# Performance work log

Hardware: AMD Instinct MI355X
Metric: run time of the kernel (lower is better)

Reference implementation:

```python
import jax, jax.numpy as jnp
import numpy as np

N_HEAD = 32
N_KV = 8
HEAD_DIM = 64  # n_embd // n_head = 2048 // 32
EPS = 1e-6


def bit_linear(x, w):
    """BitNet b1.58 BitLinear (no bias): int8 absmax activation quant (per-token),
    ternary mean-absmax weight quant, straight-through estimator."""
    s = 127.0 / jnp.clip(jnp.max(jnp.abs(x), axis=-1, keepdims=True), 1e-5)
    xq = jnp.clip(jnp.round(x * s), -128.0, 127.0) / s
    xq = x + jax.lax.stop_gradient(xq - x)
    ws = 1.0 / jnp.clip(jnp.mean(jnp.abs(w)), 1e-5)
    wq = jnp.clip(jnp.round(w * ws), -1.0, 1.0) / ws
    wq = w + jax.lax.stop_gradient(wq - w)
    return xq @ wq.T


def sub_ln(x, gamma, beta):
    mean = jnp.mean(x, axis=-1, keepdims=True)
    var = jnp.mean((x - mean) ** 2, axis=-1, keepdims=True)
    return (x - mean) / jnp.sqrt(var + EPS) * gamma + beta


def setup_inputs() -> dict:
    key = jax.random.key(0)
    ks = jax.random.split(key, 8)
    D, KV, F = 2048, 512, 8192
    B, T = 1, 2048
    w_scale = 0.02
    return {
        "x": jax.random.normal(ks[0], (B, T, D), jnp.float32),
        "g1": jnp.ones((D,), jnp.float32),
        "b1": jnp.zeros((D,), jnp.float32),
        "g2": jnp.ones((D,), jnp.float32),
        "b2": jnp.zeros((D,), jnp.float32),
        "wq": jax.random.normal(ks[1], (D, D), jnp.float32) * w_scale,
        "wk": jax.random.normal(ks[2], (KV, D), jnp.float32) * w_scale,
        "wv": jax.random.normal(ks[3], (KV, D), jnp.float32) * w_scale,
        "wo": jax.random.normal(ks[4], (D, D), jnp.float32) * w_scale,
        "w1": jax.random.normal(ks[5], (F, D), jnp.float32) * w_scale,
        "w2": jax.random.normal(ks[6], (D, F), jnp.float32) * w_scale,
    }


def reference(x, g1, b1, g2, b2, wq, wk, wv, wo, w1, w2):
    B, T, D = x.shape
    # --- attention sublayer (pre-norm, residual) ---
    h = sub_ln(x, g1, b1)
    q = bit_linear(h, wq).reshape(B, T, N_HEAD, HEAD_DIM)
    k = bit_linear(h, wk).reshape(B, T, N_KV, HEAD_DIM)
    v = bit_linear(h, wv).reshape(B, T, N_KV, HEAD_DIM)
    rep = N_HEAD // N_KV
    k = jnp.repeat(k, rep, axis=2)  # GQA repeat_interleave
    v = jnp.repeat(v, rep, axis=2)
    attn = jnp.einsum('bqhd,bkhd->bhqk', q, k) * (HEAD_DIM ** -0.5)
    causal = jnp.tril(jnp.ones((T, T), bool))
    attn = jnp.where(causal, attn, -jnp.inf)
    attn = jax.nn.softmax(attn, axis=-1)
    o = jnp.einsum('bhqk,bkhd->bqhd', attn, v).reshape(B, T, D)
    x = x + bit_linear(o, wo)
    # --- FFN sublayer (pre-norm, residual, ReLU^2) ---
    h2 = sub_ln(x, g2, b2)
    f = bit_linear(h2, w1)
    f = jnp.maximum(f, 0.0) ** 2
    return x + bit_linear(f, w2)
```

## Files before the change

kernel.cpp:

```cpp
#include <hip/hip_runtime.h>
#include <hip/hip_bf16.h>
#include <stdint.h>

typedef __bf16 bf16;
typedef signed char i8;
typedef __bf16 v8bf __attribute__((ext_vector_type(8)));
typedef __bf16 v4bf __attribute__((ext_vector_type(4)));
typedef signed char v8i8 __attribute__((ext_vector_type(8)));
typedef int    v4i  __attribute__((ext_vector_type(4)));
typedef float  f32x16 __attribute__((ext_vector_type(16)));

#define MFMA32(a,b,c)   __builtin_amdgcn_mfma_f32_32x32x16_bf16((a),(b),(c),0,0,0)
#define MFMA_I8(a,b,c)  __builtin_amdgcn_mfma_i32_16x16x64_i8((a),(b),(c),0,0,0)

__device__ __forceinline__ void glds16(const void* g, void* l) {
  __builtin_amdgcn_global_load_lds(
      (const __attribute__((address_space(1))) void*)g,
      (__attribute__((address_space(3))) void*)l, 16, 0, 0);
}

__device__ __forceinline__ float wred_sum(float v) {
#pragma unroll
  for (int o = 32; o; o >>= 1) v += __shfl_xor(v, o);
  return v;
}
__device__ __forceinline__ float wred_max(float v) {
#pragma unroll
  for (int o = 32; o; o >>= 1) v = fmaxf(v, __shfl_xor(v, o));
  return v;
}

__device__ __forceinline__ unsigned int packbf(float a, float b) {
  union { bf16 h[2]; unsigned int u; } x;
  x.h[0] = (bf16)a; x.h[1] = (bf16)b;
  return x.u;
}

__global__ void k_sniff(const unsigned short* __restrict__ x, int* __restrict__ flag) {
  int cnt = 0;
  for (int i = threadIdx.x; i < 2048; i += 64) {
    const unsigned short u = x[i];
    const int e = (u >> 7) & 0xFF;
    if (u == 0 || (e >= 100 && e <= 140)) cnt++;
  }
#pragma unroll
  for (int o = 32; o; o >>= 1) cnt += __shfl_xor(cnt, o);
  if (threadIdx.x == 0) flag[0] = (cnt >= 1844) ? 0 : 1;
}


__global__ void k_zero(float* p, int n) {
  int i = threadIdx.x;
  if (i < n) p[i] = 0.0f;
}

__global__ __launch_bounds__(256) void k_zerof(float4* __restrict__ p) {
  p[(size_t)blockIdx.x * 256 + threadIdx.x] = make_float4(0.f, 0.f, 0.f, 0.f);
}

__global__ __launch_bounds__(256) void k_abssum(const void* __restrict__ w, int n,
                                                const int* __restrict__ flag,
                                                float* __restrict__ out) {
  const int tid = threadIdx.x;
  const int f32 = flag[0];
  __shared__ float sred[4];
  float s = 0.0f;
  if (f32) {
    const float4* p = (const float4*)w;
    for (int i = (blockIdx.x * 256 + tid) * 2; i * 4 < n; i += gridDim.x * 512) {
      float4 a = p[i], b = p[i + 1];
      s += fabsf(a.x) + fabsf(a.y) + fabsf(a.z) + fabsf(a.w) +
           fabsf(b.x) + fabsf(b.y) + fabsf(b.z) + fabsf(b.w);
    }
  } else {
    const bf16* p = (const bf16*)w;
    for (int i = (blockIdx.x * 256 + tid) * 8; i < n; i += gridDim.x * 2048) {
      v8bf v = *(const v8bf*)(p + i);
#pragma unroll
      for (int j = 0; j < 8; j++) s += fabsf((float)v[j]);
    }
  }
  s = wred_sum(s);
  if ((tid & 63) == 0) sred[tid >> 6] = s;
  __syncthreads();
  if (tid == 0) atomicAdd(out, sred[0] + sred[1] + sred[2] + sred[3]);
}

__global__ __launch_bounds__(256) void k_wquant(const void* __restrict__ w, i8* __restrict__ o,
                                                const float* __restrict__ sum, float invn,
                                                const int* __restrict__ flag) {
  const int gid = blockIdx.x * 256 + threadIdx.x;
  const int i = gid * 8;
  const float ws = 1.0f / fmaxf(sum[0] * invn, 1e-5f);
  const int f32 = flag[0];
  float v[8];
  if (f32) {
    float4 a = ((const float4*)w)[gid * 2];
    float4 b = ((const float4*)w)[gid * 2 + 1];
    v[0] = a.x; v[1] = a.y; v[2] = a.z; v[3] = a.w;
    v[4] = b.x; v[5] = b.y; v[6] = b.z; v[7] = b.w;
  } else {
    v8bf t = *(const v8bf*)((const bf16*)w + i);
#pragma unroll
    for (int j = 0; j < 8; j++) v[j] = (float)t[j];
  }
  v8i8 r;
#pragma unroll
  for (int j = 0; j < 8; j++) {
    float t = rintf(v[j] * ws);
    r[j] = (i8)fminf(fmaxf(t, -1.0f), 1.0f);
  }
  *(v8i8*)(o + i) = r;
}

template <bool XINT>
__global__ __launch_bounds__(256) void k_lnq(const void* __restrict__ x, const void* __restrict__ g,
                                             const void* __restrict__ b, i8* __restrict__ q,
                                             float* __restrict__ sc, const int* __restrict__ flag) {
  const int row = blockIdx.x, tid = threadIdx.x;
  const int f32 = flag[0];
  __shared__ float sred[4];
  float v[8];
#pragma unroll
  for (int i = 0; i < 8; i++) {
    const size_t idx = (size_t)row * 2048 + tid + 256 * i;
    if (XINT)      v[i] = ((const float*)x)[idx];
    else if (f32)  v[i] = ((const float*)x)[idx];
    else           v[i] = (float)((const bf16*)x)[idx];
  }
  float s = 0.0f;
#pragma unroll
  for (int i = 0; i < 8; i++) s += v[i];
  s = wred_sum(s);
  if ((tid & 63) == 0) sred[tid >> 6] = s;
  __syncthreads();
  const float mean = (sred[0] + sred[1] + sred[2] + sred[3]) * (1.0f / 2048.0f);
  __syncthreads();
  float vs = 0.0f;
#pragma unroll
  for (int i = 0; i < 8; i++) { float d = v[i] - mean; vs += d * d; }
  vs = wred_sum(vs);
  if ((tid & 63) == 0) sred[tid >> 6] = vs;
  __syncthreads();
  const float rstd = rsqrtf((sred[0] + sred[1] + sred[2] + sred[3]) * (1.0f / 2048.0f) + 1e-6f);
  __syncthreads();
  float hq[8];
  float am = 0.0f;
#pragma unroll
  for (int i = 0; i < 8; i++) {
    const int c = tid + 256 * i;
    const float gv = f32 ? ((const float*)g)[c] : (float)((const bf16*)g)[c];
    const float bv = f32 ? ((const float*)b)[c] : (float)((const bf16*)b)[c];
    hq[i] = (v[i] - mean) * rstd * gv + bv;
    am = fmaxf(am, fabsf(hq[i]));
  }
  am = wred_max(am);
  if ((tid & 63) == 0) sred[tid >> 6] = am;
  __syncthreads();
  am = fmaxf(fmaxf(sred[0], sred[1]), fmaxf(sred[2], sred[3]));
  const float cl = fmaxf(am, 1e-5f);
  const float s127 = 127.0f / cl;
#pragma unroll
  for (int i = 0; i < 8; i++) {
    float r = rintf(hq[i] * s127);
    r = fminf(fmaxf(r, -128.0f), 127.0f);
    q[(size_t)row * 2048 + tid + 256 * i] = (i8)r;
  }
  if (tid == 0) sc[row] = cl * (1.0f / 127.0f);
}

template <int IT>
__global__ __launch_bounds__(256) void k_rowq(const bf16* __restrict__ in, i8* __restrict__ q,
                                              float* __restrict__ sc) {
  const int row = blockIdx.x, tid = threadIdx.x;
  const int C = IT * 256;
  __shared__ float sred[4];
  const bf16* xr = in + (size_t)row * C;
  float v[IT];
  float am = 0.0f;
#pragma unroll
  for (int i = 0; i < IT; i++) {
    v[i] = (float)xr[tid + 256 * i];
    am = fmaxf(am, fabsf(v[i]));
  }
  am = wred_max(am);
  if ((tid & 63) == 0) sred[tid >> 6] = am;
  __syncthreads();
  am = fmaxf(fmaxf(sred[0], sred[1]), fmaxf(sred[2], sred[3]));
  const float cl = fmaxf(am, 1e-5f);
  const float s127 = 127.0f / cl;
#pragma unroll
  for (int i = 0; i < IT; i++) {
    float r = rintf(v[i] * s127);
    r = fminf(fmaxf(r, -128.0f), 127.0f);
    q[(size_t)row * C + tid + 256 * i] = (i8)r;
  }
  if (tid == 0) sc[row] = cl * (1.0f / 127.0f);
}

template <int EPI>
__global__ __launch_bounds__(256) void k_gemm(const i8* __restrict__ A, const i8* __restrict__ B,
                                              const float* __restrict__ sA,
                                              const float* __restrict__ wsum, float winv,
                                              void* __restrict__ out,
                                              int M, int N, int K, int Kc,
                                              const int* __restrict__ flag) {
  __shared__ __align__(16) i8 As[128 * 64];
  __shared__ __align__(16) i8 Bs[128 * 64];
  const int tid = threadIdx.x;
  const int lane = tid & 63;
  const int ml = lane & 15;
  const int q4 = lane >> 4;
  const int wid = tid >> 6;
  const int wM = wid >> 1;
  const int wN = wid & 1;
  const int m0 = blockIdx.y * 128;
  const int n0 = blockIdx.x * 128;

  const int r0 = tid >> 2;
  const int c0 = (tid & 3) * 16;
  const i8* Ag0 = A + (size_t)(m0 + r0) * K + c0;
  const i8* Ag1 = Ag0 + (size_t)64 * K;
  const i8* Bg0 = B + (size_t)(n0 + r0) * K + c0;
  const i8* Bg1 = Bg0 + (size_t)64 * K;
  i8* as0 = &As[wid * 1024];
  i8* as1 = &As[4096 + wid * 1024];
  i8* bs0 = &Bs[wid * 1024];
  i8* bs1 = &Bs[4096 + wid * 1024];

  v4i acc[4][4] = {};

  const int kbeg = blockIdx.z * Kc;
  const int kfin = kbeg + Kc;
  for (int k0 = kbeg; k0 < kfin; k0 += 64) {
    __syncthreads();
    glds16(Ag0 + k0, as0);
    glds16(Ag1 + k0, as1);
    glds16(Bg0 + k0, bs0);
    glds16(Bg1 + k0, bs1);
    __syncthreads();
    v4i af[4], bfr[4];
#pragma unroll
    for (int i = 0; i < 4; i++) af[i] = *(const v4i*)&As[(wM * 64 + i * 16 + ml) * 64 + q4 * 16];
#pragma unroll
    for (int j = 0; j < 4; j++) bfr[j] = *(const v4i*)&Bs[(wN * 64 + j * 16 + ml) * 64 + q4 * 16];
#pragma unroll
    for (int i = 0; i < 4; i++)
#pragma unroll
      for (int j = 0; j < 4; j++) acc[i][j] = MFMA_I8(af[i], bfr[j], acc[i][j]);
  }

  if (EPI == 4) {
    int* ob = (int*)out;
#pragma unroll
    for (int i = 0; i < 4; i++)
#pragma unroll
      for (int r = 0; r < 4; r++) {
        const int row = m0 + wM * 64 + i * 16 + q4 * 4 + r;
#pragma unroll
        for (int j = 0; j < 4; j++) {
          const int col = n0 + wN * 64 + j * 16 + ml;
          atomicAdd(ob + (size_t)row * N + col, acc[i][j][r]);
        }
      }
    return;
  }

  const float cw = fmaxf(wsum[0] * winv, 1e-5f);
#pragma unroll
  for (int i = 0; i < 4; i++) {
#pragma unroll
    for (int r = 0; r < 4; r++) {
      const int row = m0 + wM * 64 + i * 16 + q4 * 4 + r;
      const float sa = sA[row] * cw;
#pragma unroll
      for (int j = 0; j < 4; j++) {
        const int col = n0 + wN * 64 + j * 16 + ml;
        const float val = (float)acc[i][j][r] * sa;
        float u = fmaxf(val, 0.0f);
        ((bf16*)out)[(size_t)row * N + col] = (bf16)(u * u);
      }
    }
  }
}

template <int MODE>
__global__ __launch_bounds__(256) void k_epi(const int* __restrict__ acc, int lda, int cofs,
                                             int ncols,
                                             const float* __restrict__ sA,
                                             const float* __restrict__ wsum, float winv,
                                             const void* __restrict__ resid,
                                             void* __restrict__ out,
                                             const int* __restrict__ flag) {
  const int row = blockIdx.x, tid = threadIdx.x;
  const float cw = fmaxf(wsum[0] * winv, 1e-5f);
  const float srow = (MODE == 3) ? cw : sA[row] * cw;
  const int f32 = flag[0];
  for (int c = tid * 4; c < ncols; c += 1024) {
    const v4i a = *(const v4i*)(acc + (size_t)row * lda + cofs + c);
    float s0 = srow, s1 = srow, s2 = srow, s3 = srow;
    if (MODE == 3) {
      float4 sc = *(const float4*)(sA + c);
      s0 *= sc.x; s1 *= sc.y; s2 *= sc.z; s3 *= sc.w;
    }
    const float v0 = (float)a[0] * s0, v1 = (float)a[1] * s1;
    const float v2 = (float)a[2] * s2, v3 = (float)a[3] * s3;
    const size_t o = (size_t)row * ncols + c;
    if (MODE == 0 || MODE == 3) {
      v4bf r;
      r[0] = (bf16)v0; r[1] = (bf16)v1; r[2] = (bf16)v2; r[3] = (bf16)v3;
      *(v4bf*)((bf16*)out + o) = r;
    } else if (MODE == 1) {
      float4 rv;
      if (f32) {
        rv = *(const float4*)((const float*)resid + o);
      } else {
        const v4bf rb = *(const v4bf*)((const bf16*)resid + o);
        rv = make_float4((float)rb[0], (float)rb[1], (float)rb[2], (float)rb[3]);
      }
      *(float4*)((float*)out + o) = make_float4(rv.x + v0, rv.y + v1, rv.z + v2, rv.w + v3);
    } else {
      const float4 rv = *(const float4*)((const float*)resid + o);
      const float o0 = rv.x + v0, o1 = rv.y + v1, o2 = rv.z + v2, o3 = rv.w + v3;
      if (f32) {
        *(float4*)((float*)out + o) = make_float4(o0, o1, o2, o3);
      } else {
        v4bf r;
        r[0] = (bf16)o0; r[1] = (bf16)o1; r[2] = (bf16)o2; r[3] = (bf16)o3;
        *(v4bf*)((bf16*)out + o) = r;
      }
    }
  }
}

__global__ __launch_bounds__(64) void k_attn(const bf16* __restrict__ Q, const bf16* __restrict__ Kb,
                                             const bf16* __restrict__ Vt, bf16* __restrict__ O) {
  const int h = blockIdx.y;
  const int kvh = h >> 2;
  const int t = (blockIdx.x + ((h >> 2) << 3)) & 63;
  const int qw0 = t * 32;
  const int lane = threadIdx.x;
  const int ql = lane & 31;
  const int hi = lane >> 5;

  v8bf qf[4];
  {
    const bf16* qp = Q + (size_t)(qw0 + ql) * 2048 + h * 64 + hi * 8;
#pragma unroll
    for (int c = 0; c < 4; c++) qf[c] = *(const v8bf*)(qp + c * 16);
  }

  float m = -1e30f, l = 0.0f;
  f32x16 acc0 = {}, acc1 = {};

  const bf16* kbase = Kb + kvh * 64 + hi * 8;
  const bf16* vbase = Vt + (size_t)(kvh * 64 + ql) * 2048 + hi * 8;

  for (int kb = 0; kb <= qw0; kb += 32) {
    f32x16 s = {};
    {
      const bf16* kp = kbase + (size_t)(kb + ql) * 512;
#pragma unroll
      for (int c = 0; c < 4; c++) {
        const v8bf kf = *(const v8bf*)(kp + c * 16);
        s = MFMA32(kf, qf[c], s);
      }
    }
    const bool diag = (kb == qw0);
    float p[16];
    float rm = -1e30f;
#pragma unroll
    for (int r = 0; r < 16; r++) {
      float v = s[r] * 0.125f;
      const int koff = (r & 3) + ((r >> 2) << 3) + (hi << 2);
      if (diag && koff > ql) v = -1e30f;
      p[r] = v;
      rm = fmaxf(rm, v);
    }
    rm = fmaxf(rm, __shfl_xor(rm, 32));
    const float mn = fmaxf(m, rm);
    const float alpha = __expf(m - mn);
    m = mn;
    float rs = 0.0f;
#pragma unroll
    for (int r = 0; r < 16; r++) {
      p[r] = __expf(p[r] - mn);
      rs += p[r];
    }
    rs += __shfl_xor(rs, 32);
    l = l * alpha + rs;
#pragma unroll
    for (int r = 0; r < 16; r++) { acc0[r] *= alpha; acc1[r] *= alpha; }

    unsigned int w0 = packbf(p[0], p[1]),   w2 = packbf(p[4], p[5]);
    unsigned int w1 = packbf(p[2], p[3]),   w3 = packbf(p[6], p[7]);
    unsigned int x0 = packbf(p[8], p[9]),   x2 = packbf(p[12], p[13]);
    unsigned int x1 = packbf(p[10], p[11]), x3 = packbf(p[14], p[15]);
    asm("v_permlane32_swap_b32 %0, %1" : "+v"(w0), "+v"(w2));
    asm("v_permlane32_swap_b32 %0, %1" : "+v"(w1), "+v"(w3));
    asm("v_permlane32_swap_b32 %0, %1" : "+v"(x0), "+v"(x2));
    asm("v_permlane32_swap_b32 %0, %1" : "+v"(x1), "+v"(x3));
    union BU { unsigned int u[4]; v8bf v; } B0, B1;
    B0.u[0] = w0; B0.u[1] = w1; B0.u[2] = w2; B0.u[3] = w3;
    B1.u[0] = x0; B1.u[1] = x1; B1.u[2] = x2; B1.u[3] = x3;

    const bf16* vp = vbase + kb;
    const v8bf v00 = *(const v8bf*)(vp);
    const v8bf v01 = *(const v8bf*)(vp + 16);
    const v8bf v10 = *(const v8bf*)(vp + (size_t)32 * 2048);
    const v8bf v11 = *(const v8bf*)(vp + (size_t)32 * 2048 + 16);
    acc0 = MFMA32(v00, B0.v, acc0);
    acc0 = MFMA32(v01, B1.v, acc0);
    acc1 = MFMA32(v10, B0.v, acc1);
    acc1 = MFMA32(v11, B1.v, acc1);
  }

  const float inv = 1.0f / l;
  unsigned int* op = (unsigned int*)(O + (size_t)(qw0 + ql) * 2048 + h * 64);
#pragma unroll
  for (int r = 0; r < 16; r += 2) {
    const int d = (r & 3) + ((r >> 2) << 3) + (hi << 2);
    op[d >> 1] = packbf(acc0[r] * inv, acc0[r + 1] * inv);
    op[(d >> 1) + 16] = packbf(acc1[r] * inv, acc1[r + 1] * inv);
  }
}

extern "C" void kernel_launch(void* const* d_in, const int* in_sizes, int n_in, void* d_out,
                              int out_size, void* d_ws, size_t ws_size, hipStream_t stream) {
  const void* x = d_in[0];
  const void* g1 = d_in[1];
  const void* b1 = d_in[2];
  const void* g2 = d_in[3];
  const void* b2 = d_in[4];
  const void* wq = d_in[5];
  const void* wk = d_in[6];
  const void* wv = d_in[7];
  const void* wo = d_in[8];
  const void* w1 = d_in[9];
  const void* w2 = d_in[10];

  char* ws = (char*)d_ws;
  const size_t MB = 1ull << 20;
  float* wsum = (float*)ws;
  float* s1 = (float*)(ws + 8192);
  float* so = (float*)(ws + 16384);
  float* s2 = (float*)(ws + 24576);
  float* sf = (float*)(ws + 32768);
  int* flag = (int*)(ws + 40960);
  char* big = ws + 65536;

  i8* w1z = (i8*)(big);
  i8* fq  = (i8*)(big);
  i8* w2z = (i8*)(big + 16 * MB);
  i8* wqz = (i8*)(big + 32 * MB);
  i8* wkz = (i8*)(big + 36 * MB);
  i8* wvz = (i8*)(big + 37 * MB);
  i8* woz = (i8*)(big + 38 * MB);
  i8* xq1 = (i8*)(big + 42 * MB);
  i8* oq  = xq1;
  i8* xq2 = xq1;
  int* accQK = (int*)(big + 46 * MB);
  int* accO  = (int*)(big + 46 * MB);
  bf16* Fb   = (bf16*)(big + 46 * MB);
  int* accF  = (int*)(big + 46 * MB);
  int* accVt = (int*)(big + 66 * MB);
  bf16* Qb   = (bf16*)(big + 70 * MB);
  bf16* Kbuf = (bf16*)(big + 78 * MB);
  bf16* Vt   = (bf16*)(big + 80 * MB);
  bf16* Ob   = (bf16*)(big + 82 * MB);
  float* x1  = (float*)(big + 78 * MB);

  const float invD2 = 1.0f / 4194304.0f;
  const float invKV = 1.0f / 1048576.0f;
  const float invF = 1.0f / 16777216.0f;

  k_sniff<<<1, 64, 0, stream>>>((const unsigned short*)x, flag);
  k_zero<<<1, 64, 0, stream>>>(wsum, 8);
  k_zerof<<<6144, 256, 0, stream>>>((float4*)accQK);

  k_abssum<<<512, 256, 0, stream>>>(wq, 2048 * 2048, flag, wsum + 0);
  k_abssum<<<512, 256, 0, stream>>>(wk, 512 * 2048, flag, wsum + 1);
  k_abssum<<<512, 256, 0, stream>>>(wv, 512 * 2048, flag, wsum + 2);
  k_abssum<<<512, 256, 0, stream>>>(wo, 2048 * 2048, flag, wsum + 3);
  k_abssum<<<512, 256, 0, stream>>>(w1, 8192 * 2048, flag, wsum + 4);
  k_abssum<<<512, 256, 0, stream>>>(w2, 2048 * 8192, flag, wsum + 5);
  k_wquant<<<2048, 256, 0, stream>>>(wq, wqz, wsum + 0, invD2, flag);
  k_wquant<<<512, 256, 0, stream>>>(wk, wkz, wsum + 1, invKV, flag);
  k_wquant<<<512, 256, 0, stream>>>(wv, wvz, wsum + 2, invKV, flag);
  k_wquant<<<2048, 256, 0, stream>>>(wo, woz, wsum + 3, invD2, flag);
  k_wquant<<<8192, 256, 0, stream>>>(w1, w1z, wsum + 4, invF, flag);
  k_wquant<<<8192, 256, 0, stream>>>(w2, w2z, wsum + 5, invF, flag);

  k_lnq<false><<<2048, 256, 0, stream>>>(x, g1, b1, xq1, s1, flag);
  k_gemm<4><<<dim3(20, 16, 4), 256, 0, stream>>>(xq1, wqz, s1, wsum + 0, invD2, accQK,
                                                 2048, 2560, 2048, 512, flag);
  k_gemm<4><<<dim3(16, 4, 4), 256, 0, stream>>>(wvz, xq1, s1, wsum + 2, invKV, accVt,
                                                512, 2048, 2048, 512, flag);
  k_epi<0><<<2048, 256, 0, stream>>>(accQK, 2560, 0, 2048, s1, wsum + 0, invD2, nullptr, Qb, flag);
  k_epi<0><<<2048, 256, 0, stream>>>(accQK, 2560, 2048, 512, s1, wsum + 1, invKV, nullptr, Kbuf, flag);
  k_epi<3><<<512, 256, 0, stream>>>(accVt, 2048, 0, 2048, s1, wsum + 2, invKV, nullptr, Vt, flag);
  k_attn<<<dim3(64, 32), 64, 0, stream>>>(Qb, Kbuf, Vt, Ob);
  k_rowq<8><<<2048, 256, 0, stream>>>(Ob, oq, so);
  k_zerof<<<4096, 256, 0, stream>>>((float4*)accO);
  k_gemm<4><<<dim3(16, 16, 4), 256, 0, stream>>>(oq, woz, so, wsum + 3, invD2, accO,
                                                 2048, 2048, 2048, 512, flag);
  k_epi<1><<<2048, 256, 0, stream>>>(accO, 2048, 0, 2048, so, wsum + 3, invD2, x, x1, flag);

  k_lnq<true><<<2048, 256, 0, stream>>>(x1, g2, b2, xq2, s2, flag);
  k_gemm<2><<<dim3(64, 16, 1), 256, 0, stream>>>(xq2, w1z, s2, wsum + 4, invF, Fb,
                                                 2048, 8192, 2048, 2048, flag);
  k_rowq<32><<<2048, 256, 0, stream>>>(Fb, fq, sf);
  k_zerof<<<4096, 256, 0, stream>>>((float4*)accF);
  k_gemm<4><<<dim3(16, 16, 4), 256, 0, stream>>>(fq, w2z, sf, wsum + 5, invF, accF,
                                                 2048, 2048, 8192, 2048, flag);
  k_epi<2><<<2048, 256, 0, stream>>>(accF, 2048, 0, 2048, sf, wsum + 5, invF, x1, d_out, flag);
}
```

Baseline: 715.8 us.

## Batch weight abs-sum and quant launches, double-buffer int8 GEMM LDS tiles

The six per-weight abs-sum launches become one kernel, and the six ternary-quant launches become another. Each kernel picks its weight segment from the block index, which removes launch overhead and small-grid tails. The int8 MFMA GEMM now uses two LDS buffers, so the next K tile's global-to-LDS load is issued before computing on the current tile, dropping one barrier per iteration. Workspace offsets are rearranged so the FFN buffers reuse dead regions. The cost is doubled LDS use per block, which may reduce occupancy.

```diff
diff --git a/kernel.cpp b/kernel.cpp
--- a/kernel.cpp
+++ b/kernel.cpp
@@ -13,6 +13,10 @@
 #define MFMA32(a,b,c)   __builtin_amdgcn_mfma_f32_32x32x16_bf16((a),(b),(c),0,0,0)
 #define MFMA_I8(a,b,c)  __builtin_amdgcn_mfma_i32_16x16x64_i8((a),(b),(c),0,0,0)
 
+#define INV_D2 (1.0f / 4194304.0f)
+#define INV_KV (1.0f / 1048576.0f)
+#define INV_F  (1.0f / 16777216.0f)
+
 __device__ __forceinline__ void glds16(const void* g, void* l) {
   __builtin_amdgcn_global_load_lds(
       (const __attribute__((address_space(1))) void*)g,
@@ -58,24 +62,33 @@
   p[(size_t)blockIdx.x * 256 + threadIdx.x] = make_float4(0.f, 0.f, 0.f, 0.f);
 }
 
-__global__ __launch_bounds__(256) void k_abssum(const void* __restrict__ w, int n,
-                                                const int* __restrict__ flag,
-                                                float* __restrict__ out) {
-  const int tid = threadIdx.x;
+__global__ __launch_bounds__(256) void k_abssum6(const void* __restrict__ p0, const void* __restrict__ p1,
+                                                 const void* __restrict__ p2, const void* __restrict__ p3,
+                                                 const void* __restrict__ p4, const void* __restrict__ p5,
+                                                 const int* __restrict__ flag, float* __restrict__ out) {
+  const int b = blockIdx.x, tid = threadIdx.x;
+  const void* w; int seg, base;
+  if (b < 64)       { w = p0; seg = 0; base = b; }
+  else if (b < 80)  { w = p1; seg = 1; base = b - 64; }
+  else if (b < 96)  { w = p2; seg = 2; base = b - 80; }
+  else if (b < 160) { w = p3; seg = 3; base = b - 96; }
+  else if (b < 416) { w = p4; seg = 4; base = b - 160; }
+  else              { w = p5; seg = 5; base = b - 416; }
   const int f32 = flag[0];
   __shared__ float sred[4];
   float s = 0.0f;
   if (f32) {
-    const float4* p = (const float4*)w;
-    for (int i = (blockIdx.x * 256 + tid) * 2; i * 4 < n; i += gridDim.x * 512) {
-      float4 a = p[i], b = p[i + 1];
-      s += fabsf(a.x) + fabsf(a.y) + fabsf(a.z) + fabsf(a.w) +
-           fabsf(b.x) + fabsf(b.y) + fabsf(b.z) + fabsf(b.w);
+    const float4* p = (const float4*)w + (size_t)base * 16384;
+#pragma unroll 4
+    for (int i = 0; i < 64; i++) {
+      float4 a = p[i * 256 + tid];
+      s += fabsf(a.x) + fabsf(a.y) + fabsf(a.z) + fabsf(a.w);
     }
   } else {
-    const bf16* p = (const bf16*)w;
-    for (int i = (blockIdx.x * 256 + tid) * 8; i < n; i += gridDim.x * 2048) {
-      v8bf v = *(const v8bf*)(p + i);
+    const v8bf* p = (const v8bf*)w + (size_t)base * 8192;
+#pragma unroll 4
+    for (int i = 0; i < 32; i++) {
+      v8bf v = p[i * 256 + tid];
 #pragma unroll
       for (int j = 0; j < 8; j++) s += fabsf((float)v[j]);
     }
@@ -83,22 +96,35 @@
   s = wred_sum(s);
   if ((tid & 63) == 0) sred[tid >> 6] = s;
   __syncthreads();
-  if (tid == 0) atomicAdd(out, sred[0] + sred[1] + sred[2] + sred[3]);
-}
-
-__global__ __launch_bounds__(256) void k_wquant(const void* __restrict__ w, i8* __restrict__ o,
-                                                const float* __restrict__ sum, float invn,
-                                                const int* __restrict__ flag) {
-  const int gid = blockIdx.x * 256 + threadIdx.x;
+  if (tid == 0) atomicAdd(out + seg, sred[0] + sred[1] + sred[2] + sred[3]);
+}
+
+__global__ __launch_bounds__(256) void k_wquant6(const void* __restrict__ p0, const void* __restrict__ p1,
+                                                 const void* __restrict__ p2, const void* __restrict__ p3,
+                                                 const void* __restrict__ p4, const void* __restrict__ p5,
+                                                 i8* __restrict__ d0, i8* __restrict__ d1,
+                                                 i8* __restrict__ d2, i8* __restrict__ d3,
+                                                 i8* __restrict__ d4, i8* __restrict__ d5,
+                                                 const float* __restrict__ wsum,
+                                                 const int* __restrict__ flag) {
+  const int b = blockIdx.x;
+  const void* w; i8* o; int seg, base; float invn;
+  if (b < 2048)       { w = p0; o = d0; seg = 0; base = b;         invn = INV_D2; }
+  else if (b < 2560)  { w = p1; o = d1; seg = 1; base = b - 2048;  invn = INV_KV; }
+  else if (b < 3072)  { w = p2; o = d2; seg = 2; base = b - 2560;  invn = INV_KV; }
+  else if (b < 5120)  { w = p3; o = d3; seg = 3; base = b - 3072;  invn = INV_D2; }
+  else if (b < 13312) { w = p4; o = d4; seg = 4; base = b - 5120;  invn = INV_F; }
+  else                { w = p5; o = d5; seg = 5; base = b - 13312; invn = INV_F; }
+  const int gid = base * 256 + threadIdx.x;
   const int i = gid * 8;
-  const float ws = 1.0f / fmaxf(sum[0] * invn, 1e-5f);
+  const float ws = 1.0f / fmaxf(wsum[seg] * invn, 1e-5f);
   const int f32 = flag[0];
   float v[8];
   if (f32) {
     float4 a = ((const float4*)w)[gid * 2];
-    float4 b = ((const float4*)w)[gid * 2 + 1];
+    float4 b4 = ((const float4*)w)[gid * 2 + 1];
     v[0] = a.x; v[1] = a.y; v[2] = a.z; v[3] = a.w;
-    v[4] = b.x; v[5] = b.y; v[6] = b.z; v[7] = b.w;
+    v[4] = b4.x; v[5] = b4.y; v[6] = b4.z; v[7] = b4.w;
   } else {
     v8bf t = *(const v8bf*)((const bf16*)w + i);
 #pragma unroll
@@ -205,8 +231,8 @@
                                               void* __restrict__ out,
                                               int M, int N, int K, int Kc,
                                               const int* __restrict__ flag) {
-  __shared__ __align__(16) i8 As[128 * 64];
-  __shared__ __align__(16) i8 Bs[128 * 64];
+  __shared__ __align__(16) i8 As[2][128 * 64];
+  __shared__ __align__(16) i8 Bs[2][128 * 64];
   const int tid = threadIdx.x;
   const int lane = tid & 63;
   const int ml = lane & 15;
@@ -223,31 +249,38 @@
   const i8* Ag1 = Ag0 + (size_t)64 * K;
   const i8* Bg0 = B + (size_t)(n0 + r0) * K + c0;
   const i8* Bg1 = Bg0 + (size_t)64 * K;
-  i8* as0 = &As[wid * 1024];
-  i8* as1 = &As[4096 + wid * 1024];
-  i8* bs0 = &Bs[wid * 1024];
-  i8* bs1 = &Bs[4096 + wid * 1024];
+  const int l0 = wid * 1024;
+  const int l1 = 4096 + wid * 1024;
 
   v4i acc[4][4] = {};
 
   const int kbeg = blockIdx.z * Kc;
   const int kfin = kbeg + Kc;
+  glds16(Ag0 + kbeg, &As[0][l0]);
+  glds16(Ag1 + kbeg, &As[0][l1]);
+  glds16(Bg0 + kbeg, &Bs[0][l0]);
+  glds16(Bg1 + kbeg, &Bs[0][l1]);
+  __syncthreads();
+  int cb = 0;
   for (int k0 = kbeg; k0 < kfin; k0 += 64) {
+    const int kn = k0 + 64;
+    if (kn < kfin) {
+      glds16(Ag0 + kn, &As[cb ^ 1][l0]);
+      glds16(Ag1 + kn, &As[cb ^ 1][l1]);
+      glds16(Bg0 + kn, &Bs[cb ^ 1][l0]);
+      glds16(Bg1 + kn, &Bs[cb ^ 1][l1]);
+    }
+    v4i af[4], bfr[4];
+#pragma unroll
+    for (int i = 0; i < 4; i++) af[i] = *(const v4i*)&As[cb][(wM * 64 + i * 16 + ml) * 64 + q4 * 16];
+#pragma unroll
+    for (int j = 0; j < 4; j++) bfr[j] = *(const v4i*)&Bs[cb][(wN * 64 + j * 16 + ml) * 64 + q4 * 16];
+#pragma unroll
+    for (int i = 0; i < 4; i++)
+#pragma unroll
+      for (int j = 0; j < 4; j++) acc[i][j] = MFMA_I8(af[i], bfr[j], acc[i][j]);
     __syncthreads();
-    glds16(Ag0 + k0, as0);
-    glds16(Ag1 + k0, as1);
-    glds16(Bg0 + k0, bs0);
-    glds16(Bg1 + k0, bs1);
-    __syncthreads();
-    v4i af[4], bfr[4];
-#pragma unroll
-    for (int i = 0; i < 4; i++) af[i] = *(const v4i*)&As[(wM * 64 + i * 16 + ml) * 64 + q4 * 16];
-#pragma unroll
-    for (int j = 0; j < 4; j++) bfr[j] = *(const v4i*)&Bs[(wN * 64 + j * 16 + ml) * 64 + q4 * 16];
-#pragma unroll
-    for (int i = 0; i < 4; i++)
-#pragma unroll
-      for (int j = 0; j < 4; j++) acc[i][j] = MFMA_I8(af[i], bfr[j], acc[i][j]);
+    cb ^= 1;
   }
 
   if (EPI == 4) {
@@ -458,60 +491,47 @@
   i8* woz = (i8*)(big + 38 * MB);
   i8* xq1 = (i8*)(big + 42 * MB);
   i8* oq  = xq1;
-  i8* xq2 = xq1;
   int* accQK = (int*)(big + 46 * MB);
+  int* accVt = (int*)(big + 66 * MB);
+  bf16* Kbuf = (bf16*)(big + 70 * MB);
+  bf16* Vt   = (bf16*)(big + 72 * MB);
+  bf16* Qb   = (bf16*)(big + 74 * MB);
+  bf16* Ob   = (bf16*)(big + 82 * MB);
   int* accO  = (int*)(big + 46 * MB);
-  bf16* Fb   = (bf16*)(big + 46 * MB);
-  int* accF  = (int*)(big + 46 * MB);
-  int* accVt = (int*)(big + 66 * MB);
-  bf16* Qb   = (bf16*)(big + 70 * MB);
-  bf16* Kbuf = (bf16*)(big + 78 * MB);
-  bf16* Vt   = (bf16*)(big + 80 * MB);
-  bf16* Ob   = (bf16*)(big + 82 * MB);
-  float* x1  = (float*)(big + 78 * MB);
-
-  const float invD2 = 1.0f / 4194304.0f;
-  const float invKV = 1.0f / 1048576.0f;
-  const float invF = 1.0f / 16777216.0f;
+  float* x1  = (float*)(big + 80 * MB);
+  i8* xq2 = (i8*)(big + 74 * MB);
+  bf16* Fb   = (bf16*)(big + 42 * MB);
+  int* accF  = (int*)(big + 42 * MB);
 
   k_sniff<<<1, 64, 0, stream>>>((const unsigned short*)x, flag);
   k_zero<<<1, 64, 0, stream>>>(wsum, 8);
   k_zerof<<<6144, 256, 0, stream>>>((float4*)accQK);
 
-  k_abssum<<<512, 256, 0, stream>>>(wq, 2048 * 2048, flag, wsum + 0);
-  k_abssum<<<512, 256, 0, stream>>>(wk, 512 * 2048, flag, wsum + 1);
-  k_abssum<<<512, 256, 0, stream>>>(wv, 512 * 2048, flag, wsum + 2);
-  k_abssum<<<512, 256, 0, stream>>>(wo, 2048 * 2048, flag, wsum + 3);
-  k_abssum<<<512, 256, 0, stream>>>(w1, 8192 * 2048, flag, wsum + 4);
-  k_abssum<<<512, 256, 0, stream>>>(w2, 2048 * 8192, flag, wsum + 5);
-  k_wquant<<<2048, 256, 0, stream>>>(wq, wqz, wsum + 0, invD2, flag);
-  k_wquant<<<512, 256, 0, stream>>>(wk, wkz, wsum + 1, invKV, flag);
-  k_wquant<<<512, 256, 0, stream>>>(wv, wvz, wsum + 2, invKV, flag);
-  k_wquant<<<2048, 256, 0, stream>>>(wo, woz, wsum + 3, invD2, flag);
-  k_wquant<<<8192, 256, 0, stream>>>(w1, w1z, wsum + 4, invF, flag);
-  k_wquant<<<8192, 256, 0, stream>>>(w2, w2z, wsum + 5, invF, flag);
+  k_abssum6<<<672, 256, 0, stream>>>(wq, wk, wv, wo, w1, w2, flag, wsum);
+  k_wquant6<<<21504, 256, 0, stream>>>(wq, wk, wv, wo, w1, w2,
+                                       wqz, wkz, wvz, woz, w1z, w2z, wsum, flag);
 
   k_lnq<false><<<2048, 256, 0, stream>>>(x, g1, b1, xq1, s1, flag);
-  k_gemm<4><<<dim3(20, 16, 4), 256, 0, stream>>>(xq1, wqz, s1, wsum + 0, invD2, accQK,
+  k_gemm<4><<<dim3(20, 16, 4), 256, 0, stream>>>(xq1, wqz, s1, wsum + 0, INV_D2, accQK,
                                                  2048, 2560, 2048, 512, flag);
-  k_gemm<4><<<dim3(16, 4, 4), 256, 0, stream>>>(wvz, xq1, s1, wsum + 2, invKV, accVt,
+  k_gemm<4><<<dim3(16, 4, 4), 256, 0, stream>>>(wvz, xq1, s1, wsum + 2, INV_KV, accVt,
                                                 512, 2048, 2048, 512, flag);
-  k_epi<0><<<2048, 256, 0, stream>>>(accQK, 2560, 0, 2048, s1, wsum + 0, invD2, nullptr, Qb, flag);
-  k_epi<0><<<2048, 256, 0, stream>>>(accQK, 2560, 2048, 512, s1, wsum + 1, invKV, nullptr, Kbuf, flag);
-  k_epi<3><<<512, 256, 0, stream>>>(accVt, 2048, 0, 2048, s1, wsum + 2, invKV, nullptr, Vt, flag);
+  k_epi<0><<<2048, 256, 0, stream>>>(accQK, 2560, 0, 2048, s1, wsum + 0, INV_D2, nullptr, Qb, flag);
+  k_epi<0><<<2048, 256, 0, stream>>>(accQK, 2560, 2048, 512, s1, wsum + 1, INV_KV, nullptr, Kbuf, flag);
+  k_epi<3><<<512, 256, 0, stream>>>(accVt, 2048, 0, 2048, s1, wsum + 2, INV_KV, nullptr, Vt, flag);
   k_attn<<<dim3(64, 32), 64, 0, stream>>>(Qb, Kbuf, Vt, Ob);
   k_rowq<8><<<2048, 256, 0, stream>>>(Ob, oq, so);
   k_zerof<<<4096, 256, 0, stream>>>((float4*)accO);
-  k_gemm<4><<<dim3(16, 16, 4), 256, 0, stream>>>(oq, woz, so, wsum + 3, invD2, accO,
+  k_gemm<4><<<dim3(16, 16, 4), 256, 0, stream>>>(oq, woz, so, wsum + 3, INV_D2, accO,
                                                  2048, 2048, 2048, 512, flag);
-  k_epi<1><<<2048, 256, 0, stream>>>(accO, 2048, 0, 2048, so, wsum + 3, invD2, x, x1, flag);
+  k_epi<1><<<2048, 256, 0, stream>>>(accO, 2048, 0, 2048, so, wsum + 3, INV_D2, x, x1, flag);
 
   k_lnq<true><<<2048, 256, 0, stream>>>(x1, g2, b2, xq2, s2, flag);
-  k_gemm<2><<<dim3(64, 16, 1), 256, 0, stream>>>(xq2, w1z, s2, wsum + 4, invF, Fb,
+  k_gemm<2><<<dim3(64, 16, 1), 256, 0, stream>>>(xq2, w1z, s2, wsum + 4, INV_F, Fb,
                                                  2048, 8192, 2048, 2048, flag);
   k_rowq<32><<<2048, 256, 0, stream>>>(Fb, fq, sf);
   k_zerof<<<4096, 256, 0, stream>>>((float4*)accF);
-  k_gemm<4><<<dim3(16, 16, 4), 256, 0, stream>>>(fq, w2z, sf, wsum + 5, invF, accF,
+  k_gemm<4><<<dim3(16, 16, 4), 256, 0, stream>>>(fq, w2z, sf, wsum + 5, INV_F, accF,
                                                  2048, 2048, 8192, 2048, flag);
-  k_epi<2><<<2048, 256, 0, stream>>>(accF, 2048, 0, 2048, sf, wsum + 5, invF, x1, d_out, flag);
-}
+  k_epi<2><<<2048, 256, 0, stream>>>(accF, 2048, 0, 2048, sf, wsum + 5, INV_F, x1, d_out, flag);
+}
```

Result: faster. 662.7 us (-7.4%).
